# Performance work log

Measured on AMD Instinct MI355X. Metric: run time of the kernel, lower is better.

The kernel has to match this reference:

```python
import jax, jax.numpy as jnp
import numpy as np

NUM_GRAPHS = 64


def setup_inputs() -> dict:
    key = jax.random.key(0)
    ks = jax.random.split(key, 8)
    N, E, D_IN, D_H = 50000, 800000, 128, 256
    x = jax.random.uniform(ks[0], (N, D_IN), dtype=jnp.float32)
    edge_index = jax.random.randint(ks[1], (2, E), 0, N, dtype=jnp.int64)
    batch = jnp.sort(jax.random.randint(ks[2], (N,), 0, NUM_GRAPHS, dtype=jnp.int64))
    s = 1.0 / np.sqrt(D_IN)
    s2 = 1.0 / np.sqrt(D_H)
    W1_rel = jax.random.normal(ks[3], (D_IN, D_H), dtype=jnp.float32) * s
    W1_root = jax.random.normal(ks[4], (D_IN, D_H), dtype=jnp.float32) * s
    b1 = jnp.zeros((D_H,), jnp.float32)
    W2_rel = jax.random.normal(ks[5], (D_H, D_H), dtype=jnp.float32) * s2
    W2_root = jax.random.normal(ks[6], (D_H, D_H), dtype=jnp.float32) * s2
    b2 = jnp.zeros((D_H,), jnp.float32)
    return {"x": x, "edge_index": edge_index, "batch": batch,
            "W1_rel": W1_rel, "W1_root": W1_root, "b1": b1,
            "W2_rel": W2_rel, "W2_root": W2_root, "b2": b2}


def reference(x, edge_index, batch, W1_rel, W1_root, b1, W2_rel, W2_root, b2):
    N = x.shape[0]
    src, dst = edge_index[0], edge_index[1]

    # handcrafted features: per-label fraction of total feature mass + log(graph_size)
    graph_size = jnp.sum(x)
    handcrafted = jnp.concatenate([jnp.sum(x, axis=0) / graph_size,
                                   jnp.log(graph_size)[None]])

    def graph_conv(h, W_rel, W_root, b):
        # PyG GraphConv (aggr='add'): out_i = W_rel @ sum_{j->i} h_j + W_root @ h_i + b
        agg = jax.ops.segment_sum(h[src], dst, num_segments=N)  # [N, d]
        return agg @ W_rel + h @ W_root + b

    h = jax.nn.relu(graph_conv(x, W1_rel, W1_root, b1))
    # layers 2..num_layers share the same weights (module instance reused in original)
    for _ in range(2):
        h = jax.nn.relu(graph_conv(h, W2_rel, W2_root, b2))

    # global_mean_pool over batch ids
    counts = jax.ops.segment_sum(jnp.ones((N,), h.dtype), batch, num_segments=NUM_GRAPHS)
    pooled = jax.ops.segment_sum(h, batch, num_segments=NUM_GRAPHS)
    pooled = pooled / jnp.maximum(counts, 1.0)[:, None]
    return pooled, handcrafted
```

## Files before the change

kernel.cpp:

```cpp
#include <hip/hip_runtime.h>
#include <hip/hip_bf16.h>
#include <string.h>

#define NN 50000
#define NE 800000
#define DIN 128
#define DH 256
#define NG 64
#define PSPLIT 32

typedef short bf16x8 __attribute__((ext_vector_type(8)));
typedef float f32x4 __attribute__((ext_vector_type(4)));

__device__ __forceinline__ float bf2f(__hip_bfloat16 v) { return __bfloat162float(v); }
__device__ __forceinline__ float bfbits(unsigned int lo16) {
  unsigned int u = lo16 << 16;
  float f;
  memcpy(&f, &u, 4);
  return f;
}
__device__ __forceinline__ unsigned int packbf2(float x, float y) {
  __hip_bfloat16 bx = __float2bfloat16(x), by = __float2bfloat16(y);
  unsigned short ux, uy;
  memcpy(&ux, &bx, 2);
  memcpy(&uy, &by, 2);
  return (unsigned int)ux | ((unsigned int)uy << 16);
}

__device__ __forceinline__ float loadF(const void* p, long i, int fbf) {
  return fbf ? bf2f(((const __hip_bfloat16*)p)[i]) : ((const float*)p)[i];
}
__device__ __forceinline__ void storeF(void* p, long i, float v, int fbf) {
  if (fbf) ((__hip_bfloat16*)p)[i] = __float2bfloat16(v);
  else ((float*)p)[i] = v;
}
__device__ __forceinline__ int loadI(const void* p, long i, int i64) {
  return i64 ? (int)((const long long*)p)[i] : ((const int*)p)[i];
}

__device__ __forceinline__ int lb_batch(const void* batch, int i64, int target) {
  int lo = 0, hi = NN;
  while (lo < hi) {
    int mid = (lo + hi) >> 1;
    if (loadI(batch, mid, i64) < target) lo = mid + 1;
    else hi = mid;
  }
  return lo;
}

__global__ void k_detect(const void* x, const void* ei, int* flags) {
  __shared__ int s_f32sig, s_i32sig;
  if (threadIdx.x == 0) { s_f32sig = 0; s_i32sig = 0; }
  __syncthreads();
  int t = threadIdx.x;
  const unsigned short* u = (const unsigned short*)x;
  int f = 0;
  for (int i = 2 * t; i < 8192; i += 512) if (u[i] >= 0x4000) f = 1;
  const unsigned int* w = (const unsigned int*)ei;
  int g = 0;
  for (int i = 2 * t + 1; i < 8192; i += 512) if (w[i] != 0u) g = 1;
  if (f) atomicOr(&s_f32sig, 1);
  if (g) atomicOr(&s_i32sig, 1);
  __syncthreads();
  if (t == 0) { flags[0] = s_f32sig ? 0 : 1; flags[1] = s_i32sig ? 0 : 1; }
}

__global__ void k_zero(int* __restrict__ p, int n) {
  int i = blockIdx.x * blockDim.x + threadIdx.x;
  int stride = gridDim.x * blockDim.x;
  for (; i < n; i += stride) p[i] = 0;
}

__global__ __launch_bounds__(256) void k_prep(
    const void* __restrict__ x, __hip_bfloat16* __restrict__ xb,
    float* __restrict__ colsum, const int* __restrict__ flags) {
  int fbf = flags[0];
  int t = threadIdx.x;
  int lane16 = t & 15;
  int rowoff = t >> 4;
  float acc[8] = {};
  for (int r = blockIdx.x * 16 + rowoff; r < NN; r += gridDim.x * 16) {
    uint4 o;
    if (fbf) {
      uint4 v = ((const uint4*)x)[(long)r * 16 + lane16];
      acc[0] += bfbits(v.x & 0xffffu); acc[1] += bfbits(v.x >> 16);
      acc[2] += bfbits(v.y & 0xffffu); acc[3] += bfbits(v.y >> 16);
      acc[4] += bfbits(v.z & 0xffffu); acc[5] += bfbits(v.z >> 16);
      acc[6] += bfbits(v.w & 0xffffu); acc[7] += bfbits(v.w >> 16);
      o = v;
    } else {
      float4 a = ((const float4*)x)[(long)r * 32 + lane16 * 2];
      float4 b = ((const float4*)x)[(long)r * 32 + lane16 * 2 + 1];
      acc[0] += a.x; acc[1] += a.y; acc[2] += a.z; acc[3] += a.w;
      acc[4] += b.x; acc[5] += b.y; acc[6] += b.z; acc[7] += b.w;
      o.x = packbf2(a.x, a.y); o.y = packbf2(a.z, a.w);
      o.z = packbf2(b.x, b.y); o.w = packbf2(b.z, b.w);
    }
    ((uint4*)xb)[(long)r * 16 + lane16] = o;
  }
  __shared__ float s[16][DIN];
#pragma unroll
  for (int k = 0; k < 8; ++k) s[rowoff][lane16 * 8 + k] = acc[k];
  __syncthreads();
  if (t < DIN) {
    float v = 0.f;
#pragma unroll
    for (int ro = 0; ro < 16; ++ro) v += s[ro][t];
    atomicAdd(&colsum[t], v);
  }
}

__global__ void k_handcrafted(const float* __restrict__ colsum, void* __restrict__ out,
                              const int* __restrict__ flags) {
  __shared__ float s[DIN];
  int fbf = flags[0];
  int t = threadIdx.x;
  s[t] = colsum[t];
  __syncthreads();
  for (int off = DIN / 2; off > 0; off >>= 1) {
    if (t < off) s[t] += s[t + off];
    __syncthreads();
  }
  float g = s[0];
  storeF(out, NG * DH + t, colsum[t] / g, fbf);
  if (t == 0) storeF(out, NG * DH + DIN, logf(g), fbf);
}

__global__ void k_pack_w(const void* __restrict__ Wrel, const void* __restrict__ Wroot,
                         const void* __restrict__ bias, __hip_bfloat16* __restrict__ pack,
                         float* __restrict__ biasf, const int* __restrict__ flags, int K) {
  int fbf = flags[0];
  int KS = K >> 5;
  int total = 2 * K * DH;
  int i = blockIdx.x * blockDim.x + threadIdx.x;
  int stride = gridDim.x * blockDim.x;
  for (int p = i; p < total; p += stride) {
    int m = p / (K * DH);
    int r = p % (K * DH);
    int j = r & 7;
    int l = (r >> 3) & 63;
    int q2 = r >> 9;
    int ks = q2 % KS;
    int ct = q2 / KS;
    int kk = ks * 32 + (l >> 4) * 8 + j;
    int col = ct * 16 + (l & 15);
    const void* W = m ? Wroot : Wrel;
    pack[p] = __float2bfloat16(loadF(W, (long)kk * DH + col, fbf));
  }
  if (i < DH) biasf[i] = loadF(bias, i, fbf);
}

__global__ void k_deg(const void* __restrict__ ei, int* __restrict__ cnt,
                      const int* __restrict__ flags) {
  int i64 = flags[1];
  int e = blockIdx.x * blockDim.x + threadIdx.x;
  int stride = gridDim.x * blockDim.x;
  for (; e < NE; e += stride) {
    int d = loadI(ei, (long)NE + e, i64);
    d = min(max(d, 0), NN - 1);
    atomicAdd(&cnt[d], 1);
  }
}

#define SCAN_B 256
__global__ void k_scan1(const int* __restrict__ cnt, int* __restrict__ rowptr,
                        int* __restrict__ bsum) {
  __shared__ int s[SCAN_B];
  int b = blockIdx.x, t = threadIdx.x;
  int i = b * SCAN_B + t;
  int v = (i < NN) ? cnt[i] : 0;
  s[t] = v;
  __syncthreads();
  for (int off = 1; off < SCAN_B; off <<= 1) {
    int xv = (t >= off) ? s[t - off] : 0;
    __syncthreads();
    s[t] += xv;
    __syncthreads();
  }
  if (i < NN) rowptr[i] = s[t] - v;
  if (t == SCAN_B - 1) bsum[b] = s[t];
}

__global__ void k_scan2(int* __restrict__ bsum, int nb) {
  __shared__ int s[SCAN_B];
  int t = threadIdx.x;
  int v = (t < nb) ? bsum[t] : 0;
  s[t] = v;
  __syncthreads();
  for (int off = 1; off < SCAN_B; off <<= 1) {
    int xv = (t >= off) ? s[t - off] : 0;
    __syncthreads();
    s[t] += xv;
    __syncthreads();
  }
  if (t < nb) bsum[t] = s[t] - v;
}

__global__ void k_scan3(int* __restrict__ rowptr, const int* __restrict__ bsum) {
  int i = blockIdx.x * blockDim.x + threadIdx.x;
  int stride = gridDim.x * blockDim.x;
  for (; i < NN; i += stride) rowptr[i] += bsum[i >> 8];
  if (blockIdx.x == 0 && threadIdx.x == 0) rowptr[NN] = NE;
}

__global__ void k_fill(const void* __restrict__ ei, const int* __restrict__ rowptr,
                       int* __restrict__ cur, int* __restrict__ srcs,
                       const int* __restrict__ flags) {
  int i64 = flags[1];
  int e = blockIdx.x * blockDim.x + threadIdx.x;
  int stride = gridDim.x * blockDim.x;
  for (; e < NE; e += stride) {
    int s = loadI(ei, e, i64);
    int d = loadI(ei, (long)NE + e, i64);
    s = min(max(s, 0), NN - 1);
    d = min(max(d, 0), NN - 1);
    int p = atomicAdd(&cur[d], 1);
    srcs[rowptr[d] + p] = s;
  }
}

template <int K>
__global__ __launch_bounds__(256, 4) void k_fused(
    const int* __restrict__ rowptr, const int* __restrict__ srcs,
    const __hip_bfloat16* __restrict__ hin,
    const __hip_bfloat16* __restrict__ Wpack, const float* __restrict__ bias,
    __hip_bfloat16* __restrict__ out) {
  constexpr int KS = K >> 5;
  constexpr int LROW = K + 8;
  __shared__ short agg[32 * LROW];
  int lane = threadIdx.x & 63;
  int wave = threadIdx.x >> 6;
  int row0 = blockIdx.x * 32;

  for (int s = 0; s < 8; ++s) {
    int lr = wave * 8 + s;
    int node = row0 + lr;
    float a0 = 0.f, a1 = 0.f, a2 = 0.f, a3 = 0.f;
    if (node < NN) {
      int beg = rowptr[node], end = rowptr[node + 1];
      int i = beg;
      if constexpr (K == 256) {
        const uint2* h2 = (const uint2*)hin;
        for (; i + 7 < end; i += 8) {
          uint2 v[8];
#pragma unroll
          for (int u = 0; u < 8; ++u) v[u] = h2[srcs[i + u] * 64 + lane];
#pragma unroll
          for (int u = 0; u < 8; ++u) {
            a0 += bfbits(v[u].x & 0xffffu);
            a1 += bfbits(v[u].x >> 16);
            a2 += bfbits(v[u].y & 0xffffu);
            a3 += bfbits(v[u].y >> 16);
          }
        }
        for (; i < end; ++i) {
          uint2 v0 = h2[srcs[i] * 64 + lane];
          a0 += bfbits(v0.x & 0xffffu);
          a1 += bfbits(v0.x >> 16);
          a2 += bfbits(v0.y & 0xffffu);
          a3 += bfbits(v0.y >> 16);
        }
      } else {
        const unsigned int* h1 = (const unsigned int*)hin;
        for (; i + 7 < end; i += 8) {
          unsigned int v[8];
#pragma unroll
          for (int u = 0; u < 8; ++u) v[u] = h1[srcs[i + u] * 64 + lane];
#pragma unroll
          for (int u = 0; u < 8; ++u) {
            a0 += bfbits(v[u] & 0xffffu);
            a1 += bfbits(v[u] >> 16);
          }
        }
        for (; i < end; ++i) {
          unsigned int v0 = h1[srcs[i] * 64 + lane];
          a0 += bfbits(v0 & 0xffffu);
          a1 += bfbits(v0 >> 16);
        }
      }
    }
    if constexpr (K == 256) {
      uint2 o;
      o.x = packbf2(a0, a1);
      o.y = packbf2(a2, a3);
      *(uint2*)&agg[lr * LROW + lane * 4] = o;
    } else {
      *(unsigned int*)&agg[lr * LROW + lane * 2] = packbf2(a0, a1);
    }
  }
  __syncthreads();

  int m15 = lane & 15;
  int q = lane >> 4;
  const short* A2s = (const short*)hin;
  const short* Wp = (const short*)Wpack;
  const int wrootOfs = K * DH;
  f32x4 acc[2][4] = {};
#pragma unroll
  for (int ks = 0; ks < KS; ++ks) {
    int kofs = ks * 32 + q * 8;
    bf16x8 va1[2], va2[2], b1[4], b2[4];
#pragma unroll
    for (int mt = 0; mt < 2; ++mt) {
      int lr = mt * 16 + m15;
      va1[mt] = *(const bf16x8*)&agg[lr * LROW + kofs];
      int r = row0 + lr;
      if (r > NN - 1) r = NN - 1;
      va2[mt] = *(const bf16x8*)(A2s + r * K + kofs);
    }
#pragma unroll
    for (int ct = 0; ct < 4; ++ct) {
      int gct = wave * 4 + ct;
      const short* base = Wp + ((gct * KS + ks) * 64 + lane) * 8;
      b1[ct] = *(const bf16x8*)(base);
      b2[ct] = *(const bf16x8*)(base + wrootOfs);
    }
#pragma unroll
    for (int mt = 0; mt < 2; ++mt)
#pragma unroll
      for (int ct = 0; ct < 4; ++ct) {
        acc[mt][ct] = __builtin_amdgcn_mfma_f32_16x16x32_bf16(va1[mt], b1[ct], acc[mt][ct], 0, 0, 0);
        acc[mt][ct] = __builtin_amdgcn_mfma_f32_16x16x32_bf16(va2[mt], b2[ct], acc[mt][ct], 0, 0, 0);
      }
  }
#pragma unroll
  for (int mt = 0; mt < 2; ++mt)
#pragma unroll
    for (int ct = 0; ct < 4; ++ct) {
      int col = (wave * 4 + ct) * 16 + m15;
      float bv = bias[col];
#pragma unroll
      for (int r = 0; r < 4; ++r) {
        int row = row0 + mt * 16 + q * 4 + r;
        if (row < NN) {
          float v = acc[mt][ct][r] + bv;
          out[row * DH + col] = __float2bfloat16(fmaxf(v, 0.f));
        }
      }
    }
}

__global__ void k_poolpart(const void* __restrict__ batch, const __hip_bfloat16* __restrict__ h,
                           float* __restrict__ pooled, const int* __restrict__ flags) {
  int i64 = flags[1];
  int g = blockIdx.x;
  int p = blockIdx.y;
  int j = threadIdx.x;
  int s = lb_batch(batch, i64, g);
  int e = lb_batch(batch, i64, g + 1);
  int len = e - s;
  if (len <= 0) return;
  int chunk = (len + PSPLIT - 1) / PSPLIT;
  int rs = s + p * chunk;
  int re = min(rs + chunk, e);
  if (rs >= re) return;
  const unsigned int* h2 = (const unsigned int*)h;
  float a0 = 0.f, a1 = 0.f;
  for (int r = rs; r < re; ++r) {
    unsigned int v = h2[(long)r * 128 + j];
    a0 += bfbits(v & 0xffffu);
    a1 += bfbits(v >> 16);
  }
  atomicAdd(&pooled[g * DH + 2 * j], a0);
  atomicAdd(&pooled[g * DH + 2 * j + 1], a1);
}

__global__ void k_poolfin(const void* __restrict__ batch, const float* __restrict__ pooled,
                          void* __restrict__ out, const int* __restrict__ flags) {
  int fbf = flags[0];
  int i64 = flags[1];
  int g = blockIdx.x;
  int j = threadIdx.x;
  int s = lb_batch(batch, i64, g);
  int e = lb_batch(batch, i64, g + 1);
  float cnt = fmaxf((float)(e - s), 1.0f);
  storeF(out, (long)g * DH + j, pooled[g * DH + j] / cnt, fbf);
}

extern "C" void kernel_launch(void* const* d_in, const int* in_sizes, int n_in,
                              void* d_out, int out_size, void* d_ws, size_t ws_size,
                              hipStream_t stream) {
  const void* x = d_in[0];
  const void* ei = d_in[1];
  const void* batch = d_in[2];
  const void* W1r = d_in[3];
  const void* W1o = d_in[4];
  const void* b1 = d_in[5];
  const void* W2r = d_in[6];
  const void* W2o = d_in[7];
  const void* b2 = d_in[8];
  void* out = d_out;

  char* w = (char*)d_ws;
  auto alloc = [&](size_t bytes) -> char* {
    char* p = w;
    w += (bytes + 255) & ~(size_t)255;
    return p;
  };
  int* flags = (int*)alloc(64);
  const int zero_n = NN + NN + DIN + NG * DH;
  int* zreg = (int*)alloc((size_t)zero_n * 4);
  int* cnt = zreg;
  int* cur = cnt + NN;
  float* colsum = (float*)(cur + NN);
  float* pooled = (float*)(colsum + DIN);
  int* rowptr = (int*)alloc((NN + 1) * 4);
  int* bsum = (int*)alloc(SCAN_B * 4);
  int* srcs = (int*)alloc((size_t)NE * 4);
  __hip_bfloat16* xb = (__hip_bfloat16*)alloc((size_t)NN * DIN * 2);
  __hip_bfloat16* hA = (__hip_bfloat16*)alloc((size_t)NN * DH * 2);
  __hip_bfloat16* hB = (__hip_bfloat16*)alloc((size_t)NN * DH * 2);
  __hip_bfloat16* wp1 = (__hip_bfloat16*)alloc((size_t)2 * DIN * DH * 2);
  __hip_bfloat16* wp2 = (__hip_bfloat16*)alloc((size_t)2 * DH * DH * 2);
  float* b1f = (float*)alloc(DH * 4);
  float* b2f = (float*)alloc(DH * 4);

  const int nblk = (NN + SCAN_B - 1) / SCAN_B;
  const int fused_grid = (NN + 31) / 32;

  k_detect<<<1, 256, 0, stream>>>(x, ei, flags);
  k_zero<<<512, 256, 0, stream>>>(zreg, zero_n);

  k_pack_w<<<64, 256, 0, stream>>>(W1r, W1o, b1, wp1, b1f, flags, DIN);
  k_pack_w<<<128, 256, 0, stream>>>(W2r, W2o, b2, wp2, b2f, flags, DH);
  k_prep<<<1024, 256, 0, stream>>>(x, xb, colsum, flags);
  k_handcrafted<<<1, 128, 0, stream>>>(colsum, out, flags);

  k_deg<<<1024, 256, 0, stream>>>(ei, cnt, flags);
  k_scan1<<<nblk, SCAN_B, 0, stream>>>(cnt, rowptr, bsum);
  k_scan2<<<1, SCAN_B, 0, stream>>>(bsum, nblk);
  k_scan3<<<256, 256, 0, stream>>>(rowptr, bsum);
  k_fill<<<1024, 256, 0, stream>>>(ei, rowptr, cur, srcs, flags);

  k_fused<DIN><<<fused_grid, 256, 0, stream>>>(rowptr, srcs, xb, wp1, b1f, hA);
  k_fused<DH><<<fused_grid, 256, 0, stream>>>(rowptr, srcs, hA, wp2, b2f, hB);
  k_fused<DH><<<fused_grid, 256, 0, stream>>>(rowptr, srcs, hB, wp2, b2f, hA);

  k_poolpart<<<dim3(NG, PSPLIT), 128, 0, stream>>>(batch, hA, pooled, flags);
  k_poolfin<<<NG, DH, 0, stream>>>(batch, pooled, out, flags);
}
```

Measured before the change: 539.2 us.

## Split fused gather-GEMM into column-sliced gather and separate MFMA GEMM

Node feature matrices are stored in a column-sliced layout: 32-column slabs for hidden features and 16-column slabs for the input features. Each layer's fused gather+GEMM kernel is split into a gather kernel and a GEMM kernel. The gather kernel handles one slice per block, so the gathered working set per slice is small enough to stay cache-resident, and it spreads edges across lanes with shuffle reductions. The cost is an extra aggregation buffer written to and read back from global memory, plus more kernel launches, in exchange for better cache locality in the random gathers.

```diff
diff --git a/kernel.cpp b/kernel.cpp
--- a/kernel.cpp
+++ b/kernel.cpp
@@ -46,6 +46,12 @@
     else hi = mid;
   }
   return lo;
+}
+
+template <int K>
+__device__ __forceinline__ int sl_addr(int r, int ks, int q) {
+  if constexpr (K == 256) return (ks * NN + r) * 32 + q * 8;
+  else return ((2 * ks + (q >> 1)) * NN + r) * 16 + (q & 1) * 8;
 }
 
 __global__ void k_detect(const void* x, const void* ei, int* flags) {
@@ -96,7 +102,7 @@
       o.x = packbf2(a.x, a.y); o.y = packbf2(a.z, a.w);
       o.z = packbf2(b.x, b.y); o.w = packbf2(b.z, b.w);
     }
-    ((uint4*)xb)[(long)r * 16 + lane16] = o;
+    ((uint4*)xb)[((long)(lane16 >> 1) * NN + r) * 2 + (lane16 & 1)] = o;
   }
   __shared__ float s[16][DIN];
 #pragma unroll
@@ -219,94 +225,103 @@
   }
 }
 
+__global__ __launch_bounds__(256) void k_gather_sl256(
+    const int* __restrict__ rowptr, const int* __restrict__ srcs,
+    const __hip_bfloat16* __restrict__ hs, __hip_bfloat16* __restrict__ aggs) {
+  int b = blockIdx.x;
+  int slice = b & 7;
+  int tile = b >> 3;
+  int wave = threadIdx.x >> 6;
+  int lane = threadIdx.x & 63;
+  int eslot = lane >> 4;
+  int cu = lane & 15;
+  const unsigned int* hsl = (const unsigned int*)hs + (size_t)slice * NN * 16;
+  unsigned int* asl = (unsigned int*)aggs + (size_t)slice * NN * 16;
+  for (int s = 0; s < 4; ++s) {
+    int node = tile * 16 + wave * 4 + s;
+    if (node >= NN) break;
+    int beg = rowptr[node], end = rowptr[node + 1];
+    float a0 = 0.f, a1 = 0.f;
+    for (int i = beg; i < end; i += 16) {
+#pragma unroll
+      for (int j = 0; j < 4; ++j) {
+        int raw = i + j * 4 + eslot;
+        int idx = raw < end ? raw : end - 1;
+        int sv = __builtin_nontemporal_load(srcs + idx);
+        unsigned int v = hsl[sv * 16 + cu];
+        v = raw < end ? v : 0u;
+        a0 += bfbits(v & 0xffffu);
+        a1 += bfbits(v >> 16);
+      }
+    }
+    a0 += __shfl_xor(a0, 16); a1 += __shfl_xor(a1, 16);
+    a0 += __shfl_xor(a0, 32); a1 += __shfl_xor(a1, 32);
+    if (lane < 16) __builtin_nontemporal_store(packbf2(a0, a1), &asl[node * 16 + cu]);
+  }
+}
+
+__global__ __launch_bounds__(256) void k_gather_sl128(
+    const int* __restrict__ rowptr, const int* __restrict__ srcs,
+    const __hip_bfloat16* __restrict__ hs, __hip_bfloat16* __restrict__ aggs) {
+  int b = blockIdx.x;
+  int slice = b & 7;
+  int tile = b >> 3;
+  int wave = threadIdx.x >> 6;
+  int lane = threadIdx.x & 63;
+  int eslot = lane >> 3;
+  int cu = lane & 7;
+  const unsigned int* hsl = (const unsigned int*)hs + (size_t)slice * NN * 8;
+  unsigned int* asl = (unsigned int*)aggs + (size_t)slice * NN * 8;
+  for (int s = 0; s < 4; ++s) {
+    int node = tile * 16 + wave * 4 + s;
+    if (node >= NN) break;
+    int beg = rowptr[node], end = rowptr[node + 1];
+    float a0 = 0.f, a1 = 0.f;
+    for (int i = beg; i < end; i += 32) {
+#pragma unroll
+      for (int j = 0; j < 4; ++j) {
+        int raw = i + j * 8 + eslot;
+        int idx = raw < end ? raw : end - 1;
+        int sv = __builtin_nontemporal_load(srcs + idx);
+        unsigned int v = hsl[sv * 8 + cu];
+        v = raw < end ? v : 0u;
+        a0 += bfbits(v & 0xffffu);
+        a1 += bfbits(v >> 16);
+      }
+    }
+    a0 += __shfl_xor(a0, 8);  a1 += __shfl_xor(a1, 8);
+    a0 += __shfl_xor(a0, 16); a1 += __shfl_xor(a1, 16);
+    a0 += __shfl_xor(a0, 32); a1 += __shfl_xor(a1, 32);
+    if (lane < 8) __builtin_nontemporal_store(packbf2(a0, a1), &asl[node * 8 + cu]);
+  }
+}
+
 template <int K>
-__global__ __launch_bounds__(256, 4) void k_fused(
-    const int* __restrict__ rowptr, const int* __restrict__ srcs,
-    const __hip_bfloat16* __restrict__ hin,
+__global__ __launch_bounds__(256, 4) void k_gemm(
+    const __hip_bfloat16* __restrict__ A1, const __hip_bfloat16* __restrict__ A2,
     const __hip_bfloat16* __restrict__ Wpack, const float* __restrict__ bias,
     __hip_bfloat16* __restrict__ out) {
   constexpr int KS = K >> 5;
-  constexpr int LROW = K + 8;
-  __shared__ short agg[32 * LROW];
   int lane = threadIdx.x & 63;
   int wave = threadIdx.x >> 6;
-  int row0 = blockIdx.x * 32;
-
-  for (int s = 0; s < 8; ++s) {
-    int lr = wave * 8 + s;
-    int node = row0 + lr;
-    float a0 = 0.f, a1 = 0.f, a2 = 0.f, a3 = 0.f;
-    if (node < NN) {
-      int beg = rowptr[node], end = rowptr[node + 1];
-      int i = beg;
-      if constexpr (K == 256) {
-        const uint2* h2 = (const uint2*)hin;
-        for (; i + 7 < end; i += 8) {
-          uint2 v[8];
-#pragma unroll
-          for (int u = 0; u < 8; ++u) v[u] = h2[srcs[i + u] * 64 + lane];
-#pragma unroll
-          for (int u = 0; u < 8; ++u) {
-            a0 += bfbits(v[u].x & 0xffffu);
-            a1 += bfbits(v[u].x >> 16);
-            a2 += bfbits(v[u].y & 0xffffu);
-            a3 += bfbits(v[u].y >> 16);
-          }
-        }
-        for (; i < end; ++i) {
-          uint2 v0 = h2[srcs[i] * 64 + lane];
-          a0 += bfbits(v0.x & 0xffffu);
-          a1 += bfbits(v0.x >> 16);
-          a2 += bfbits(v0.y & 0xffffu);
-          a3 += bfbits(v0.y >> 16);
-        }
-      } else {
-        const unsigned int* h1 = (const unsigned int*)hin;
-        for (; i + 7 < end; i += 8) {
-          unsigned int v[8];
-#pragma unroll
-          for (int u = 0; u < 8; ++u) v[u] = h1[srcs[i + u] * 64 + lane];
-#pragma unroll
-          for (int u = 0; u < 8; ++u) {
-            a0 += bfbits(v[u] & 0xffffu);
-            a1 += bfbits(v[u] >> 16);
-          }
-        }
-        for (; i < end; ++i) {
-          unsigned int v0 = h1[srcs[i] * 64 + lane];
-          a0 += bfbits(v0 & 0xffffu);
-          a1 += bfbits(v0 >> 16);
-        }
-      }
-    }
-    if constexpr (K == 256) {
-      uint2 o;
-      o.x = packbf2(a0, a1);
-      o.y = packbf2(a2, a3);
-      *(uint2*)&agg[lr * LROW + lane * 4] = o;
-    } else {
-      *(unsigned int*)&agg[lr * LROW + lane * 2] = packbf2(a0, a1);
-    }
-  }
-  __syncthreads();
-
   int m15 = lane & 15;
   int q = lane >> 4;
-  const short* A2s = (const short*)hin;
+  int row0 = blockIdx.x * 32;
+  const short* A1s = (const short*)A1;
+  const short* A2s = (const short*)A2;
   const short* Wp = (const short*)Wpack;
   const int wrootOfs = K * DH;
   f32x4 acc[2][4] = {};
 #pragma unroll
   for (int ks = 0; ks < KS; ++ks) {
-    int kofs = ks * 32 + q * 8;
-    bf16x8 va1[2], va2[2], b1[4], b2[4];
+    bf16x8 a1[2], a2[2], b1[4], b2[4];
 #pragma unroll
     for (int mt = 0; mt < 2; ++mt) {
-      int lr = mt * 16 + m15;
-      va1[mt] = *(const bf16x8*)&agg[lr * LROW + kofs];
-      int r = row0 + lr;
+      int r = row0 + mt * 16 + m15;
       if (r > NN - 1) r = NN - 1;
-      va2[mt] = *(const bf16x8*)(A2s + r * K + kofs);
+      int ad = sl_addr<K>(r, ks, q);
+      a1[mt] = *(const bf16x8*)(A1s + ad);
+      a2[mt] = *(const bf16x8*)(A2s + ad);
     }
 #pragma unroll
     for (int ct = 0; ct < 4; ++ct) {
@@ -319,8 +334,8 @@
     for (int mt = 0; mt < 2; ++mt)
 #pragma unroll
       for (int ct = 0; ct < 4; ++ct) {
-        acc[mt][ct] = __builtin_amdgcn_mfma_f32_16x16x32_bf16(va1[mt], b1[ct], acc[mt][ct], 0, 0, 0);
-        acc[mt][ct] = __builtin_amdgcn_mfma_f32_16x16x32_bf16(va2[mt], b2[ct], acc[mt][ct], 0, 0, 0);
+        acc[mt][ct] = __builtin_amdgcn_mfma_f32_16x16x32_bf16(a1[mt], b1[ct], acc[mt][ct], 0, 0, 0);
+        acc[mt][ct] = __builtin_amdgcn_mfma_f32_16x16x32_bf16(a2[mt], b2[ct], acc[mt][ct], 0, 0, 0);
       }
   }
 #pragma unroll
@@ -329,12 +344,13 @@
     for (int ct = 0; ct < 4; ++ct) {
       int col = (wave * 4 + ct) * 16 + m15;
       float bv = bias[col];
+      int slice = col >> 5, cof = col & 31;
 #pragma unroll
       for (int r = 0; r < 4; ++r) {
         int row = row0 + mt * 16 + q * 4 + r;
         if (row < NN) {
           float v = acc[mt][ct][r] + bv;
-          out[row * DH + col] = __float2bfloat16(fmaxf(v, 0.f));
+          out[(slice * NN + row) * 32 + cof] = __float2bfloat16(fmaxf(v, 0.f));
         }
       }
     }
@@ -355,9 +371,10 @@
   int re = min(rs + chunk, e);
   if (rs >= re) return;
   const unsigned int* h2 = (const unsigned int*)h;
+  int slice = j >> 4, cu = j & 15;
   float a0 = 0.f, a1 = 0.f;
   for (int r = rs; r < re; ++r) {
-    unsigned int v = h2[(long)r * 128 + j];
+    unsigned int v = h2[((long)slice * NN + r) * 16 + cu];
     a0 += bfbits(v & 0xffffu);
     a1 += bfbits(v >> 16);
   }
@@ -408,6 +425,7 @@
   int* bsum = (int*)alloc(SCAN_B * 4);
   int* srcs = (int*)alloc((size_t)NE * 4);
   __hip_bfloat16* xb = (__hip_bfloat16*)alloc((size_t)NN * DIN * 2);
+  __hip_bfloat16* aggb = (__hip_bfloat16*)alloc((size_t)NN * DH * 2);
   __hip_bfloat16* hA = (__hip_bfloat16*)alloc((size_t)NN * DH * 2);
   __hip_bfloat16* hB = (__hip_bfloat16*)alloc((size_t)NN * DH * 2);
   __hip_bfloat16* wp1 = (__hip_bfloat16*)alloc((size_t)2 * DIN * DH * 2);
@@ -416,7 +434,8 @@
   float* b2f = (float*)alloc(DH * 4);
 
   const int nblk = (NN + SCAN_B - 1) / SCAN_B;
-  const int fused_grid = (NN + 31) / 32;
+  const int gemm_grid = (NN + 31) / 32;
+  const int gat_grid = ((NN + 15) / 16) * 8;
 
   k_detect<<<1, 256, 0, stream>>>(x, ei, flags);
   k_zero<<<512, 256, 0, stream>>>(zreg, zero_n);
@@ -432,9 +451,12 @@
   k_scan3<<<256, 256, 0, stream>>>(rowptr, bsum);
   k_fill<<<1024, 256, 0, stream>>>(ei, rowptr, cur, srcs, flags);
 
-  k_fused<DIN><<<fused_grid, 256, 0, stream>>>(rowptr, srcs, xb, wp1, b1f, hA);
-  k_fused<DH><<<fused_grid, 256, 0, stream>>>(rowptr, srcs, hA, wp2, b2f, hB);
-  k_fused<DH><<<fused_grid, 256, 0, stream>>>(rowptr, srcs, hB, wp2, b2f, hA);
+  k_gather_sl128<<<gat_grid, 256, 0, stream>>>(rowptr, srcs, xb, aggb);
+  k_gemm<DIN><<<gemm_grid, 256, 0, stream>>>(aggb, xb, wp1, b1f, hA);
+  k_gather_sl256<<<gat_grid, 256, 0, stream>>>(rowptr, srcs, hA, aggb);
+  k_gemm<DH><<<gemm_grid, 256, 0, stream>>>(aggb, hA, wp2, b2f, hB);
+  k_gather_sl256<<<gat_grid, 256, 0, stream>>>(rowptr, srcs, hB, aggb);
+  k_gemm<DH><<<gemm_grid, 256, 0, stream>>>(aggb, hB, wp2, b2f, hA);
 
   k_poolpart<<<dim3(NG, PSPLIT), 128, 0, stream>>>(batch, hA, pooled, flags);
   k_poolfin<<<NG, DH, 0, stream>>>(batch, pooled, out, flags);
```

Result: slower. 685.3 us (+27.1%).
